# Optimization experiments

Hardware: AMD Instinct MI355X
Metric: run time of the kernel (lower is better)

## Reference

```python
import jax, jax.numpy as jnp
import numpy as np

D, S, L, W, H, V = 64, 64, 64, 300, 300, 50000
NEG = jnp.float32(-9999999.0)


def setup_inputs() -> dict:
    key = jax.random.key(0)
    ks = jax.random.split(key, 16)
    n = lambda k, shape, s=0.05: jax.random.normal(k, shape, dtype=jnp.float32) * s
    return {
        "word_indices": jax.random.randint(ks[0], (D, S, L), 0, V),
        "E": n(ks[1], (V, W), 0.1),
        "W_sent": n(ks[2], (H, W)), "b_sent": jnp.zeros((H,), jnp.float32),
        "W_par": n(ks[3], (H, H)), "b_par": jnp.zeros((H,), jnp.float32),
        "W_ch": n(ks[4], (H, H)), "b_ch": jnp.zeros((H,), jnp.float32),
        "w_root": n(ks[5], (H,)), "b_root": jnp.zeros((), jnp.float32),
        "root_embed": n(ks[6], (H,)),
        "W_r": n(ks[7], (H, 3 * H)), "b_r": jnp.zeros((H,), jnp.float32),
        "W_cls": n(ks[8], (2, H)), "b_cls": jnp.zeros((2,), jnp.float32),
    }


def reference(word_indices, E, W_sent, b_sent, W_par, b_par, W_ch, b_ch,
              w_root, b_root, root_embed, W_r, b_r, W_cls, b_cls):
    lrelu = lambda x: jax.nn.leaky_relu(x, 0.01)
    # Ragged pad+gather stage of the original, dense here (all lengths == L)
    word_embed = E[word_indices]                 # [D,S,L,W]
    # 0.5*(X[l-1] + reverse(reverse(X))[l-1]) == X[l-1]; LSTM outputs unused in source
    x_last = word_embed[:, :, -1, :]             # [D,S,W]
    enc = lrelu(x_last @ W_sent.T + b_sent)      # [D,S,H] sentence encodings
    # Pairwise parent-child edge scores (O(S^2) dots in the original loops)
    P = lrelu(enc @ W_par.T + b_par)             # [D,S,H]
    C = lrelu(enc @ W_ch.T + b_ch)               # [D,S,H]
    A = jnp.einsum('dih,djh->dij', P, C)         # [D,S,S]
    A = jnp.where(jnp.eye(S, dtype=bool)[None], NEG, A)
    A = jax.nn.softmax(A, axis=1)                # Softmax(dim=0) per doc: over parents i
    scores = enc @ w_root + b_root               # [D,S] root scores
    fri = jax.nn.softmax(scores, axis=1)         # Softmax(dim=0) over sentences
    # ri[i] = r_embeds([enc_i, sum_k A[k,i]*enc_k + fri_i*root, enc_i*sum_k A[i,k]])
    tmp = jnp.einsum('dki,dkh->dih', A, enc)     # [D,S,H]
    agg = tmp + fri[..., None] * root_embed      # [D,S,H]
    tmp3 = enc * A.sum(axis=2, keepdims=True)    # [D,S,H]
    ri = lrelu(jnp.concatenate([enc, agg, tmp3], axis=-1) @ W_r.T + b_r)  # [D,S,H]
    final = ri.mean(axis=1)                      # [D,H]
    out = final @ W_cls.T + b_cls                # [D,2]
    return out, A, fri
```

## Files before the change

kernel.cpp:

```cpp
#include <hip/hip_runtime.h>
#include <hip/hip_bf16.h>

#define NEG_INF (-9999999.0f)

typedef __attribute__((ext_vector_type(8))) short bf16x8;
typedef __attribute__((ext_vector_type(4))) float f32x4;
typedef unsigned short us;

__device__ __forceinline__ float b2f(us u) {
  union { unsigned int i; float f; } x; x.i = ((unsigned int)u) << 16; return x.f;
}
__device__ __forceinline__ us f2b(float f) {
  union { float f; unsigned int i; } x; x.f = f;
  unsigned int r = x.i + 0x7fffu + ((x.i >> 16) & 1u);
  return (us)(r >> 16);
}
__device__ __forceinline__ float lrelu(float v) { return v > 0.f ? v : 0.01f * v; }
__device__ __forceinline__ bf16x8 ld8(const us* p) { return *reinterpret_cast<const bf16x8*>(p); }

__global__ __launch_bounds__(256) void k_prep(const int* __restrict__ wi, const float* __restrict__ E,
    const float* __restrict__ Ws, const float* __restrict__ Wp, const float* __restrict__ Wc,
    const float* __restrict__ Wr,
    us* __restrict__ Wsb, us* __restrict__ Wpb, us* __restrict__ Wcb, us* __restrict__ Wrb,
    us* __restrict__ xg, us* __restrict__ encb, us* __restrict__ Pb, us* __restrict__ Cb,
    us* __restrict__ encTb) {
  int task = blockIdx.y;
  int gid = blockIdx.x * 256 + threadIdx.x;
  const int stride = 640 * 256;
  if (task < 3) {
    const float* src = (task == 0) ? Ws : (task == 1) ? Wp : Wc;
    us* dst = (task == 0) ? Wsb : (task == 1) ? Wpb : Wcb;
    for (int i = gid; i < 304 * 320; i += stride) {
      int r = i / 320, c = i - r * 320;
      dst[i] = (r < 300 && c < 300) ? f2b(src[r * 300 + c]) : 0;
    }
  } else if (task == 3) {
    for (int i = gid; i < 304 * 928; i += stride) {
      int r = i / 928, c = i - r * 928;
      Wrb[i] = (r < 300 && c < 900) ? f2b(Wr[r * 900 + c]) : 0;
    }
  } else if (task == 4) {
    for (int i = gid; i < 4096 * 320; i += stride) {
      int r = i / 320, c = i - r * 320;
      xg[i] = (c < 300) ? f2b(E[(long)wi[r * 64 + 63] * 300 + c]) : 0;
    }
  } else if (task == 5) {
    for (int i = gid; i < 3 * 4096 * 20; i += stride) {
      int b = i / 81920, rem = i - b * 81920;
      int r = rem / 20, c = 300 + (rem - r * 20);
      us* dst = (b == 0) ? encb : (b == 1) ? Pb : Cb;
      dst[r * 320 + c] = 0;
    }
  } else {
    for (int i = gid; i < 4 * 4096; i += stride)
      encTb[300 * 4096 + i] = 0;
  }
}

template<int NT>
__device__ __forceinline__ void sweep(const us* __restrict__ Ab, int apitch,
    const us* __restrict__ Bb, int bpitch, int m0, int nt0, int lo, int q,
    int ks0, int ksn, f32x4* acc) {
  const us* ar = Ab + (long)(m0 + lo) * apitch + 8 * q + (long)ks0 * 32;
  const us* br[NT];
#pragma unroll
  for (int t = 0; t < NT; ++t)
    br[t] = Bb + (long)((nt0 + t) * 16 + lo) * bpitch + 8 * q + (long)ks0 * 32;
  bf16x8 a0 = ld8(ar), a1 = ld8(ar + 32);
  bf16x8 b0[NT], b1[NT];
#pragma unroll
  for (int t = 0; t < NT; ++t) b0[t] = ld8(br[t]);
#pragma unroll
  for (int t = 0; t < NT; ++t) b1[t] = ld8(br[t] + 32);
  for (int ks = 0; ks < ksn - 2; ++ks) {
    bf16x8 a2 = ld8(ar + (ks + 2) * 32);
    bf16x8 b2[NT];
#pragma unroll
    for (int t = 0; t < NT; ++t) b2[t] = ld8(br[t] + (ks + 2) * 32);
#pragma unroll
    for (int t = 0; t < NT; ++t)
      acc[t] = __builtin_amdgcn_mfma_f32_16x16x32_bf16(a0, b0[t], acc[t], 0, 0, 0);
    a0 = a1; a1 = a2;
#pragma unroll
    for (int t = 0; t < NT; ++t) { b0[t] = b1[t]; b1[t] = b2[t]; }
  }
#pragma unroll
  for (int t = 0; t < NT; ++t)
    acc[t] = __builtin_amdgcn_mfma_f32_16x16x32_bf16(a0, b0[t], acc[t], 0, 0, 0);
#pragma unroll
  for (int t = 0; t < NT; ++t)
    acc[t] = __builtin_amdgcn_mfma_f32_16x16x32_bf16(a1, b1[t], acc[t], 0, 0, 0);
}

template<int NT>
__device__ __forceinline__ void epi_bf16(const f32x4* acc, const float* __restrict__ bias,
    us* __restrict__ outb, us* __restrict__ outT,
    int m0, int nt0, int lo, int q) {
#pragma unroll
  for (int t = 0; t < NT; ++t) {
    int col = (nt0 + t) * 16 + lo;
    if (col >= 300) continue;
    float bb = bias[col];
#pragma unroll
    for (int r = 0; r < 4; ++r) {
      int row = m0 + q * 4 + r;
      us h = f2b(lrelu(acc[t][r] + bb));
      outb[(long)row * 320 + col] = h;
      if (outT) outT[(long)col * 4096 + row] = h;
    }
  }
}

__global__ __launch_bounds__(256) void k_gemm_enc(const us* __restrict__ Ab,
    const us* __restrict__ Bb, const float* __restrict__ bias,
    us* __restrict__ encb, us* __restrict__ encTb) {
  int w = threadIdx.x >> 6, lane = threadIdx.x & 63;
  int lo = lane & 15, q = lane >> 4;
  int m0 = blockIdx.x * 16;
  f32x4 z = {0.f, 0.f, 0.f, 0.f};
  if (w < 3) {
    f32x4 acc[5] = {z, z, z, z, z};
    sweep<5>(Ab, 320, Bb, 320, m0, w * 5, lo, q, 0, 10, acc);
    epi_bf16<5>(acc, bias, encb, encTb, m0, w * 5, lo, q);
  } else {
    f32x4 acc[4] = {z, z, z, z};
    sweep<4>(Ab, 320, Bb, 320, m0, 15, lo, q, 0, 10, acc);
    epi_bf16<4>(acc, bias, encb, encTb, m0, 15, lo, q);
  }
}

__global__ __launch_bounds__(256) void k_gemm_pc(const us* __restrict__ Ab,
    const us* __restrict__ Wpb, const us* __restrict__ Wcb,
    const float* __restrict__ bp, const float* __restrict__ bc,
    us* __restrict__ Pb, us* __restrict__ Cb) {
  int which = blockIdx.y;
  const us* Bb = which ? Wcb : Wpb;
  const float* bias = which ? bc : bp;
  us* outb = which ? Cb : Pb;
  int w = threadIdx.x >> 6, lane = threadIdx.x & 63;
  int lo = lane & 15, q = lane >> 4;
  int m0 = blockIdx.x * 16;
  f32x4 z = {0.f, 0.f, 0.f, 0.f};
  if (w < 3) {
    f32x4 acc[5] = {z, z, z, z, z};
    sweep<5>(Ab, 320, Bb, 320, m0, w * 5, lo, q, 0, 10, acc);
    epi_bf16<5>(acc, bias, outb, (us*)nullptr, m0, w * 5, lo, q);
  } else {
    f32x4 acc[4] = {z, z, z, z};
    sweep<4>(Ab, 320, Bb, 320, m0, 15, lo, q, 0, 10, acc);
    epi_bf16<4>(acc, bias, outb, (us*)nullptr, m0, 15, lo, q);
  }
}

__global__ __launch_bounds__(256) void k_attn(
    const us* __restrict__ Pb, const us* __restrict__ Cb, const us* __restrict__ encb,
    const float* __restrict__ w_root, const float* __restrict__ b_root,
    float* __restrict__ Aout, float* __restrict__ outF,
    us* __restrict__ Atb, float* __restrict__ rsp) {
  __shared__ float Ls[64][17];
  __shared__ float pm[4][16], psum[4][16];
  __shared__ float scores[64];
  int d = blockIdx.x, jg = blockIdx.y, t = threadIdx.x;
  int w = t >> 6, lane = t & 63, lo = lane & 15, q = lane >> 4;

  {
    int rr = t >> 2, quad = t & 3;
    const us* er = encb + (long)(d * 64 + rr) * 320;
    float s = 0.f;
    for (int h = quad * 4; h + 4 <= 300; h += 16) {
      ushort4 e4 = *reinterpret_cast<const ushort4*>(er + h);
      s = fmaf(b2f(e4.x), w_root[h], s);
      s = fmaf(b2f(e4.y), w_root[h + 1], s);
      s = fmaf(b2f(e4.z), w_root[h + 2], s);
      s = fmaf(b2f(e4.w), w_root[h + 3], s);
    }
    s += __shfl_xor(s, 1);
    s += __shfl_xor(s, 2);
    if (quad == 0) scores[rr] = s + b_root[0];
  }
  __syncthreads();
  if (jg == 0 && t < 64) {
    float s = scores[t];
    float m = s;
#pragma unroll
    for (int o = 32; o > 0; o >>= 1) m = fmaxf(m, __shfl_xor(m, o, 64));
    float e = expf(s - m);
    float sum = e;
#pragma unroll
    for (int o = 32; o > 0; o >>= 1) sum += __shfl_xor(sum, o, 64);
    outF[d * 64 + t] = e / sum;
  }

  {
    const us* Pd = Pb + (long)d * 64 * 320;
    const us* Cd = Cb + (long)d * 64 * 320;
    f32x4 acc = {0.f, 0.f, 0.f, 0.f};
    sweep<1>(Pd, 320, Cd, 320, w * 16, jg, lo, q, 0, 10, &acc);
#pragma unroll
    for (int r = 0; r < 4; ++r) {
      int i = w * 16 + q * 4 + r, j = jg * 16 + lo;
      Ls[i][lo] = (i == j) ? NEG_INF : acc[r];
    }
  }
  __syncthreads();

  {
    int col = t & 15, p = t >> 4;
    if (t < 64) {
      float mx = -3.0e38f;
      for (int i = p * 16; i < p * 16 + 16; ++i) mx = fmaxf(mx, Ls[i][col]);
      pm[p][col] = mx;
    }
    __syncthreads();
    if (t < 64) {
      float gmx = fmaxf(fmaxf(pm[0][col], pm[1][col]), fmaxf(pm[2][col], pm[3][col]));
      float s = 0.f;
      for (int i = p * 16; i < p * 16 + 16; ++i) s += expf(Ls[i][col] - gmx);
      psum[p][col] = s;
    }
    __syncthreads();
    if (t < 64) {
      float gmx = fmaxf(fmaxf(pm[0][col], pm[1][col]), fmaxf(pm[2][col], pm[3][col]));
      float inv = 1.f / (psum[0][col] + psum[1][col] + psum[2][col] + psum[3][col]);
      int j = jg * 16 + col;
      float* Ad = Aout + (long)d * 4096;
      us* Atd = Atb + (long)d * 4096;
      for (int i = p * 16; i < p * 16 + 16; ++i) {
        float a = expf(Ls[i][col] - gmx) * inv;
        Ad[i * 64 + j] = a;
        Atd[j * 64 + i] = f2b(a);
        Ls[i][col] = a;
      }
    }
  }
  __syncthreads();
  if (t < 64) {
    float s = 0.f;
#pragma unroll
    for (int c = 0; c < 16; ++c) s += Ls[t][c];
    rsp[(d * 4 + jg) * 64 + t] = s;
  }
}

__global__ __launch_bounds__(256) void k_glue2(
    const us* __restrict__ Atb, const us* __restrict__ encTb, const us* __restrict__ encb,
    const float* __restrict__ outF, const float* __restrict__ rsp,
    const float* __restrict__ root, us* __restrict__ ub) {
  __shared__ float frs[64], rs[64];
  int d = blockIdx.x, g = blockIdx.y, t = threadIdx.x;
  if (t < 64) {
    frs[t] = outF[d * 64 + t];
    rs[t] = rsp[(d * 4 + 0) * 64 + t] + rsp[(d * 4 + 1) * 64 + t]
          + rsp[(d * 4 + 2) * 64 + t] + rsp[(d * 4 + 3) * 64 + t];
  }
  __syncthreads();
  int w = t >> 6, lane = t & 63, lo = lane & 15, q = lane >> 4;
  int ht = g * 4 + w;
  if (ht < 19) {
    const us* Atd = Atb + (long)d * 4096;
    bf16x8 av0[4], av1[4];
#pragma unroll
    for (int mt = 0; mt < 4; ++mt) {
      av0[mt] = ld8(Atd + (mt * 16 + lo) * 64 + 8 * q);
      av1[mt] = ld8(Atd + (mt * 16 + lo) * 64 + 32 + 8 * q);
    }
    const us* brow = encTb + (long)(ht * 16 + lo) * 4096 + d * 64 + 8 * q;
    bf16x8 bv0 = ld8(brow), bv1 = ld8(brow + 32);
    int h = ht * 16 + lo;
    float rt = (h < 300) ? root[h] : 0.f;
#pragma unroll
    for (int mt = 0; mt < 4; ++mt) {
      f32x4 acc = {0.f, 0.f, 0.f, 0.f};
      acc = __builtin_amdgcn_mfma_f32_16x16x32_bf16(av0[mt], bv0, acc, 0, 0, 0);
      acc = __builtin_amdgcn_mfma_f32_16x16x32_bf16(av1[mt], bv1, acc, 0, 0, 0);
      if (h < 300) {
#pragma unroll
        for (int r = 0; r < 4; ++r) {
          int i = mt * 16 + q * 4 + r;
          ub[(long)(d * 64 + i) * 928 + 300 + h] = f2b(acc[r] + frs[i] * rt);
        }
      }
    }
  }
  for (int idx = t; idx < 64 * 60; idx += 256) {
    int r = idx / 60, c = g * 60 + (idx - (idx / 60) * 60);
    us ev = encb[(long)(d * 64 + r) * 320 + c];
    ub[(long)(d * 64 + r) * 928 + c] = ev;
    ub[(long)(d * 64 + r) * 928 + 600 + c] = f2b(b2f(ev) * rs[r]);
  }
  if (g == 4) {
    for (int idx = t; idx < 64 * 28; idx += 256) {
      int r = idx / 28, c = 900 + (idx - r * 28);
      ub[(long)(d * 64 + r) * 928 + c] = 0;
    }
  }
}

__global__ __launch_bounds__(256) void k_gemm_ri(const us* __restrict__ Ab,
    const us* __restrict__ Bb, const float* __restrict__ bias, float* __restrict__ ri) {
  int w = threadIdx.x >> 6, lane = threadIdx.x & 63;
  int lo = lane & 15, q = lane >> 4;
  int m0 = blockIdx.x * 16;
  f32x4 z = {0.f, 0.f, 0.f, 0.f};
  if (w < 3) {
    f32x4 acc[5] = {z, z, z, z, z};
    sweep<5>(Ab, 928, Bb, 928, m0, w * 5, lo, q, 0, 29, acc);
#pragma unroll
    for (int t2 = 0; t2 < 5; ++t2) {
      int col = (w * 5 + t2) * 16 + lo;
      if (col >= 300) continue;
      float bb = bias[col];
#pragma unroll
      for (int r = 0; r < 4; ++r)
        ri[(long)(m0 + q * 4 + r) * 300 + col] = lrelu(acc[t2][r] + bb);
    }
  } else {
    f32x4 acc[4] = {z, z, z, z};
    sweep<4>(Ab, 928, Bb, 928, m0, 15, lo, q, 0, 29, acc);
#pragma unroll
    for (int t2 = 0; t2 < 4; ++t2) {
      int col = (15 + t2) * 16 + lo;
      if (col >= 300) continue;
      float bb = bias[col];
#pragma unroll
      for (int r = 0; r < 4; ++r)
        ri[(long)(m0 + q * 4 + r) * 300 + col] = lrelu(acc[t2][r] + bb);
    }
  }
}

__global__ __launch_bounds__(256) void k_final(const float* __restrict__ ri,
    const float* __restrict__ W_cls, const float* __restrict__ b_cls,
    float* __restrict__ outp) {
  __shared__ float fin[300];
  __shared__ float red[256];
  int d = blockIdx.x, t = threadIdx.x;
  for (int h = t; h < 300; h += 256) {
    float s = 0.f;
    for (int i = 0; i < 64; ++i) s += ri[((d * 64) + i) * 300 + h];
    fin[h] = s * (1.0f / 64.0f);
  }
  __syncthreads();
  for (int c2 = 0; c2 < 2; ++c2) {
    float pth = 0.f;
    for (int h = t; h < 300; h += 256) pth = fmaf(fin[h], W_cls[c2 * 300 + h], pth);
    red[t] = pth;
    __syncthreads();
    for (int o = 128; o > 0; o >>= 1) {
      if (t < o) red[t] += red[t + o];
      __syncthreads();
    }
    if (t == 0) outp[d * 2 + c2] = red[0] + b_cls[c2];
    __syncthreads();
  }
}

extern "C" void kernel_launch(void* const* d_in, const int* in_sizes, int n_in,
                              void* d_out, int out_size, void* d_ws, size_t ws_size,
                              hipStream_t stream) {
  const int*   wi     = (const int*)d_in[0];
  const float* E      = (const float*)d_in[1];
  const float* W_sent = (const float*)d_in[2];
  const float* b_sent = (const float*)d_in[3];
  const float* W_par  = (const float*)d_in[4];
  const float* b_par  = (const float*)d_in[5];
  const float* W_ch   = (const float*)d_in[6];
  const float* b_ch   = (const float*)d_in[7];
  const float* w_root = (const float*)d_in[8];
  const float* b_root = (const float*)d_in[9];
  const float* root_e = (const float*)d_in[10];
  const float* W_r    = (const float*)d_in[11];
  const float* b_r    = (const float*)d_in[12];
  const float* W_cls  = (const float*)d_in[13];
  const float* b_cls  = (const float*)d_in[14];

  us* B = (us*)d_ws;
  us* Wsb   = B;
  us* Wpb   = B + 97280;
  us* Wcb   = B + 194560;
  us* Wrb   = B + 291840;
  us* xg    = B + 573952;
  us* encb  = B + 1884672;
  us* encTb = B + 3195392;
  us* Pb    = B + 4440576;
  us* Cb    = B + 5751296;
  us* ub    = B + 7062016;
  us* Atb   = B + 10863104;
  float* rsp = (float*)(B + 11125248);
  float* ri  = (float*)(B + 11157760);

  float* outp = (float*)d_out;
  float* outA = outp + 128;
  float* outF = outp + 128 + 262144;

  k_prep<<<dim3(640, 7), 256, 0, stream>>>(wi, E, W_sent, W_par, W_ch, W_r,
                                           Wsb, Wpb, Wcb, Wrb, xg, encb, Pb, Cb, encTb);
  k_gemm_enc<<<256, 256, 0, stream>>>(xg, Wsb, b_sent, encb, encTb);
  k_gemm_pc<<<dim3(256, 2), 256, 0, stream>>>(encb, Wpb, Wcb, b_par, b_ch, Pb, Cb);
  k_attn<<<dim3(64, 4), 256, 0, stream>>>(Pb, Cb, encb, w_root, b_root,
                                          outA, outF, Atb, rsp);
  k_glue2<<<dim3(64, 5), 256, 0, stream>>>(Atb, encTb, encb, outF, rsp, root_e, ub);
  k_gemm_ri<<<256, 256, 0, stream>>>(ub, Wrb, b_r, ri);
  k_final<<<64, 256, 0, stream>>>(ri, W_cls, b_cls, outp);
}
```

Measured before the change: 191.6 us.

## Stage A tiles in LDS for GEMMs, deepen B prefetch, dedupe root scores

The three bf16 MFMA GEMM kernels now copy the block's 16-row A tile into shared memory once, so the four waves read A from LDS instead of each fetching it from global memory. The new sweep also prefetches B three k-steps ahead instead of two. In the attention kernel, only the jg==0 block computes the root scores and their softmax, which removes redundant work in the other column-group blocks. The cost is an extra staging pass, a barrier before compute, more LDS per block (about 29 KB for the ri GEMM), and more registers for the deeper B buffers.

```diff
diff --git a/kernel.cpp b/kernel.cpp
--- a/kernel.cpp
+++ b/kernel.cpp
@@ -57,6 +57,63 @@
   }
 }
 
+__device__ __forceinline__ void stage16(const us* __restrict__ g, us* lds, int units, int t) {
+  const float4* s = reinterpret_cast<const float4*>(g);
+  float4* d = reinterpret_cast<float4*>(lds);
+  for (int i = t; i < units; i += 256) d[i] = s[i];
+}
+
+template<int NT, int KP>
+__device__ __forceinline__ void sweep_lds(const us* As, const us* __restrict__ Bb,
+    int bpitch, int nt0, int lo, int q, int ksn, f32x4* acc) {
+  const us* ar = As + lo * KP + 8 * q;
+  const us* br[NT];
+#pragma unroll
+  for (int t = 0; t < NT; ++t)
+    br[t] = Bb + (long)((nt0 + t) * 16 + lo) * bpitch + 8 * q;
+  bf16x8 b0[NT], b1[NT], b2[NT];
+#pragma unroll
+  for (int t = 0; t < NT; ++t) b0[t] = ld8(br[t]);
+#pragma unroll
+  for (int t = 0; t < NT; ++t) b1[t] = ld8(br[t] + 32);
+#pragma unroll
+  for (int t = 0; t < NT; ++t) b2[t] = ld8(br[t] + 64);
+  bf16x8 a0 = *reinterpret_cast<const bf16x8*>(ar);
+  for (int ks = 0; ks < ksn - 3; ++ks) {
+    bf16x8 a1 = *reinterpret_cast<const bf16x8*>(ar + (ks + 1) * 32);
+    bf16x8 bn[NT];
+#pragma unroll
+    for (int t = 0; t < NT; ++t) bn[t] = ld8(br[t] + (ks + 3) * 32);
+#pragma unroll
+    for (int t = 0; t < NT; ++t)
+      acc[t] = __builtin_amdgcn_mfma_f32_16x16x32_bf16(a0, b0[t], acc[t], 0, 0, 0);
+    a0 = a1;
+#pragma unroll
+    for (int t = 0; t < NT; ++t) { b0[t] = b1[t]; b1[t] = b2[t]; b2[t] = bn[t]; }
+  }
+  {
+    bf16x8 a1 = *reinterpret_cast<const bf16x8*>(ar + (ksn - 2) * 32);
+#pragma unroll
+    for (int t = 0; t < NT; ++t)
+      acc[t] = __builtin_amdgcn_mfma_f32_16x16x32_bf16(a0, b0[t], acc[t], 0, 0, 0);
+    a0 = a1;
+#pragma unroll
+    for (int t = 0; t < NT; ++t) b0[t] = b1[t];
+  }
+  {
+    bf16x8 a1 = *reinterpret_cast<const bf16x8*>(ar + (ksn - 1) * 32);
+#pragma unroll
+    for (int t = 0; t < NT; ++t)
+      acc[t] = __builtin_amdgcn_mfma_f32_16x16x32_bf16(a0, b0[t], acc[t], 0, 0, 0);
+    a0 = a1;
+#pragma unroll
+    for (int t = 0; t < NT; ++t) b0[t] = b2[t];
+  }
+#pragma unroll
+  for (int t = 0; t < NT; ++t)
+    acc[t] = __builtin_amdgcn_mfma_f32_16x16x32_bf16(a0, b0[t], acc[t], 0, 0, 0);
+}
+
 template<int NT>
 __device__ __forceinline__ void sweep(const us* __restrict__ Ab, int apitch,
     const us* __restrict__ Bb, int bpitch, int m0, int nt0, int lo, int q,
@@ -114,17 +171,20 @@
 __global__ __launch_bounds__(256) void k_gemm_enc(const us* __restrict__ Ab,
     const us* __restrict__ Bb, const float* __restrict__ bias,
     us* __restrict__ encb, us* __restrict__ encTb) {
-  int w = threadIdx.x >> 6, lane = threadIdx.x & 63;
-  int lo = lane & 15, q = lane >> 4;
+  __shared__ __align__(16) us As[16 * 320];
+  int t = threadIdx.x;
   int m0 = blockIdx.x * 16;
+  stage16(Ab + (long)m0 * 320, As, 640, t);
+  __syncthreads();
+  int w = t >> 6, lane = t & 63, lo = lane & 15, q = lane >> 4;
   f32x4 z = {0.f, 0.f, 0.f, 0.f};
   if (w < 3) {
     f32x4 acc[5] = {z, z, z, z, z};
-    sweep<5>(Ab, 320, Bb, 320, m0, w * 5, lo, q, 0, 10, acc);
+    sweep_lds<5, 320>(As, Bb, 320, w * 5, lo, q, 10, acc);
     epi_bf16<5>(acc, bias, encb, encTb, m0, w * 5, lo, q);
   } else {
     f32x4 acc[4] = {z, z, z, z};
-    sweep<4>(Ab, 320, Bb, 320, m0, 15, lo, q, 0, 10, acc);
+    sweep_lds<4, 320>(As, Bb, 320, 15, lo, q, 10, acc);
     epi_bf16<4>(acc, bias, encb, encTb, m0, 15, lo, q);
   }
 }
@@ -133,21 +193,24 @@
     const us* __restrict__ Wpb, const us* __restrict__ Wcb,
     const float* __restrict__ bp, const float* __restrict__ bc,
     us* __restrict__ Pb, us* __restrict__ Cb) {
+  __shared__ __align__(16) us As[16 * 320];
   int which = blockIdx.y;
   const us* Bb = which ? Wcb : Wpb;
   const float* bias = which ? bc : bp;
   us* outb = which ? Cb : Pb;
-  int w = threadIdx.x >> 6, lane = threadIdx.x & 63;
-  int lo = lane & 15, q = lane >> 4;
+  int t = threadIdx.x;
   int m0 = blockIdx.x * 16;
+  stage16(Ab + (long)m0 * 320, As, 640, t);
+  __syncthreads();
+  int w = t >> 6, lane = t & 63, lo = lane & 15, q = lane >> 4;
   f32x4 z = {0.f, 0.f, 0.f, 0.f};
   if (w < 3) {
     f32x4 acc[5] = {z, z, z, z, z};
-    sweep<5>(Ab, 320, Bb, 320, m0, w * 5, lo, q, 0, 10, acc);
+    sweep_lds<5, 320>(As, Bb, 320, w * 5, lo, q, 10, acc);
     epi_bf16<5>(acc, bias, outb, (us*)nullptr, m0, w * 5, lo, q);
   } else {
     f32x4 acc[4] = {z, z, z, z};
-    sweep<4>(Ab, 320, Bb, 320, m0, 15, lo, q, 0, 10, acc);
+    sweep_lds<4, 320>(As, Bb, 320, 15, lo, q, 10, acc);
     epi_bf16<4>(acc, bias, outb, (us*)nullptr, m0, 15, lo, q);
   }
 }
@@ -163,7 +226,7 @@
   int d = blockIdx.x, jg = blockIdx.y, t = threadIdx.x;
   int w = t >> 6, lane = t & 63, lo = lane & 15, q = lane >> 4;
 
-  {
+  if (jg == 0) {
     int rr = t >> 2, quad = t & 3;
     const us* er = encb + (long)(d * 64 + rr) * 320;
     float s = 0.f;
@@ -177,18 +240,18 @@
     s += __shfl_xor(s, 1);
     s += __shfl_xor(s, 2);
     if (quad == 0) scores[rr] = s + b_root[0];
-  }
-  __syncthreads();
-  if (jg == 0 && t < 64) {
-    float s = scores[t];
-    float m = s;
-#pragma unroll
-    for (int o = 32; o > 0; o >>= 1) m = fmaxf(m, __shfl_xor(m, o, 64));
-    float e = expf(s - m);
-    float sum = e;
-#pragma unroll
-    for (int o = 32; o > 0; o >>= 1) sum += __shfl_xor(sum, o, 64);
-    outF[d * 64 + t] = e / sum;
+    __syncthreads();
+    if (t < 64) {
+      float sc = scores[t];
+      float m = sc;
+#pragma unroll
+      for (int o = 32; o > 0; o >>= 1) m = fmaxf(m, __shfl_xor(m, o, 64));
+      float e = expf(sc - m);
+      float sum = e;
+#pragma unroll
+      for (int o = 32; o > 0; o >>= 1) sum += __shfl_xor(sum, o, 64);
+      outF[d * 64 + t] = e / sum;
+    }
   }
 
   {
@@ -298,13 +361,16 @@
 
 __global__ __launch_bounds__(256) void k_gemm_ri(const us* __restrict__ Ab,
     const us* __restrict__ Bb, const float* __restrict__ bias, float* __restrict__ ri) {
-  int w = threadIdx.x >> 6, lane = threadIdx.x & 63;
-  int lo = lane & 15, q = lane >> 4;
+  __shared__ __align__(16) us As[16 * 928];
+  int t = threadIdx.x;
   int m0 = blockIdx.x * 16;
+  stage16(Ab + (long)m0 * 928, As, 1856, t);
+  __syncthreads();
+  int w = t >> 6, lane = t & 63, lo = lane & 15, q = lane >> 4;
   f32x4 z = {0.f, 0.f, 0.f, 0.f};
   if (w < 3) {
     f32x4 acc[5] = {z, z, z, z, z};
-    sweep<5>(Ab, 928, Bb, 928, m0, w * 5, lo, q, 0, 29, acc);
+    sweep_lds<5, 928>(As, Bb, 928, w * 5, lo, q, 29, acc);
 #pragma unroll
     for (int t2 = 0; t2 < 5; ++t2) {
       int col = (w * 5 + t2) * 16 + lo;
@@ -316,7 +382,7 @@
     }
   } else {
     f32x4 acc[4] = {z, z, z, z};
-    sweep<4>(Ab, 928, Bb, 928, m0, 15, lo, q, 0, 29, acc);
+    sweep_lds<4, 928>(As, Bb, 928, 15, lo, q, 29, acc);
 #pragma unroll
     for (int t2 = 0; t2 < 4; ++t2) {
       int col = (15 + t2) * 16 + lo;
```

Measured after the change: 189.0 us. About the same (-1.4%).
